# Kernel tuning notes

Hardware: AMD Instinct MI355X
Metric: run time of the kernel (lower is better)

## Reference

```python
import jax, jax.numpy as jnp
import numpy as np

N_NODES = 100000
N_EDGES = 1600000
IN_DIM, HID_DIM, OUT_DIM = 128, 128, 64


def setup_inputs() -> dict:
    key = jax.random.key(0)
    ks = jax.random.split(key, 8)
    x = jax.random.normal(ks[0], (N_NODES, IN_DIM), dtype=jnp.float32)
    edge_index = jax.random.randint(ks[1], (2, N_EDGES), 0, N_NODES, dtype=jnp.int64)
    s1 = 1.0 / np.sqrt(IN_DIM)
    s2 = 1.0 / np.sqrt(HID_DIM)
    return {
        "x": x,
        "edge_index": edge_index,
        "W1l": jax.random.normal(ks[2], (IN_DIM, HID_DIM), dtype=jnp.float32) * s1,
        "b1": jnp.zeros((HID_DIM,), dtype=jnp.float32),
        "W1r": jax.random.normal(ks[3], (IN_DIM, HID_DIM), dtype=jnp.float32) * s1,
        "W2l": jax.random.normal(ks[4], (HID_DIM, OUT_DIM), dtype=jnp.float32) * s2,
        "b2": jnp.zeros((OUT_DIM,), dtype=jnp.float32),
        "W2r": jax.random.normal(ks[5], (HID_DIM, OUT_DIM), dtype=jnp.float32) * s2,
    }


def _sage_conv(h, src, dst, n_nodes, Wl, bl, Wr):
    # mean-aggregate neighbor messages src -> dst, then linear + root linear
    msg = h[src]                                               # [E, d]
    summed = jax.ops.segment_sum(msg, dst, num_segments=n_nodes)
    cnt = jax.ops.segment_sum(jnp.ones((src.shape[0],), h.dtype), dst,
                              num_segments=n_nodes)
    aggr = summed / jnp.maximum(cnt, 1.0)[:, None]             # [N, d]
    return aggr @ Wl + bl + h @ Wr                             # [N, d_out]


def reference(x, edge_index, W1l, b1, W1r, W2l, b2, W2r):
    src, dst = edge_index[0], edge_index[1]
    n = x.shape[0]
    h = jax.nn.relu(_sage_conv(x, src, dst, n, W1l, b1, W1r))
    # dropout is identity in eval mode (training=False)
    return _sage_conv(h, src, dst, n, W2l, b2, W2r)
```

## Files before the change

kernel.cpp:

```cpp
#include <hip/hip_runtime.h>
#include <hip/hip_bf16.h>
#include <stdint.h>

#define N_NODES 100000
#define N_EDGES 1600000
#define IN_DIM 128
#define HID_DIM 128
#define OUT_DIM 64
#define NBUCKET 391
#define NBE 391
#define ECHUNK 4096
#define HM (NBUCKET * NBE)
#define NB_SCAN 150
#define SENTINEL N_NODES
#define PCAP 6144
#define GEMM_ROWBLKS 782
#define GEMM_GRID (GEMM_ROWBLKS * 2)

typedef __bf16 bf16x8 __attribute__((ext_vector_type(8)));
typedef float f32x4 __attribute__((ext_vector_type(4)));
typedef float f32x2 __attribute__((ext_vector_type(2)));

__device__ __forceinline__ uint16_t f_to_bf16(float f) {
    uint32_t u = __float_as_uint(f);
    u += 0x7fffu + ((u >> 16) & 1u);
    return (uint16_t)(u >> 16);
}
__device__ __forceinline__ uint32_t pack_bf16x2(float lo, float hi) {
    return (uint32_t)f_to_bf16(lo) | ((uint32_t)f_to_bf16(hi) << 16);
}


__global__ __launch_bounds__(256) void prep_k(const int* __restrict__ dst,
                                              const float* __restrict__ x,
                                              const float* __restrict__ W1l,
                                              const float* __restrict__ W1r,
                                              const float* __restrict__ W2l,
                                              const float* __restrict__ W2r,
                                              int* __restrict__ hist,
                                              uint32_t* __restrict__ xf8,
                                              uint16_t* __restrict__ wT1,
                                              uint16_t* __restrict__ wT2) {
    __shared__ int lh[NBUCKET];
    int blk = blockIdx.x, t = threadIdx.x;
    if (blk < NBE) {
        for (int i = t; i < NBUCKET; i += 256) lh[i] = 0;
        __syncthreads();
        int e0 = blk * ECHUNK;
        int e1 = e0 + ECHUNK; if (e1 > N_EDGES) e1 = N_EDGES;
        for (int e = e0 + t; e < e1; e += 256) atomicAdd(&lh[dst[e] >> 8], 1);
        __syncthreads();
        for (int i = t; i < NBUCKET; i += 256) hist[i * NBE + blk] = lh[i];
    } else if (blk < NBE + 6250) {
        int i = (blk - NBE) * 256 + t;
        if (blk == NBE && t < 32) xf8[N_NODES * 32 + t] = 0u;
        if (i >= N_NODES * IN_DIM / 8) return;
        const float4* xv = (const float4*)x;
        float4 v0 = xv[2 * i], v1 = xv[2 * i + 1];
        int p0 = __builtin_amdgcn_cvt_pk_fp8_f32(v0.x, v0.y, 0, false);
        p0 = __builtin_amdgcn_cvt_pk_fp8_f32(v0.z, v0.w, p0, true);
        int p1 = __builtin_amdgcn_cvt_pk_fp8_f32(v1.x, v1.y, 0, false);
        p1 = __builtin_amdgcn_cvt_pk_fp8_f32(v1.z, v1.w, p1, true);
        uint2 w2; w2.x = (uint32_t)p0; w2.y = (uint32_t)p1;
        ((uint2*)xf8)[i] = w2;
    } else {
        int i = (blk - NBE - 6250) * 256 + t;
        if (i < 128 * 256) {
            int n = i >> 8, k = i & 255;
            float v = (k < 128) ? W1l[k * 128 + n] : W1r[(k - 128) * 128 + n];
            wT1[i] = f_to_bf16(v);
        } else {
            int j = i - 128 * 256;
            if (j < 128 * 128) {
                int n = j >> 7, k = j & 127;
                float v = (n < 64) ? W2l[k * 64 + n] : W2r[k * 64 + (n - 64)];
                wT2[j] = f_to_bf16(v);
            }
        }
    }
}


__global__ void scan1_k(int* __restrict__ data, int* __restrict__ partials, int n) {
    __shared__ int sm[256];
    int tid = threadIdx.x;
    int base = blockIdx.x * 1024 + tid * 4;
    int v0 = 0, v1 = 0, v2 = 0, v3 = 0;
    if (base + 0 < n) v0 = data[base + 0];
    if (base + 1 < n) v1 = data[base + 1];
    if (base + 2 < n) v2 = data[base + 2];
    if (base + 3 < n) v3 = data[base + 3];
    int tot = v0 + v1 + v2 + v3;
    sm[tid] = tot;
    __syncthreads();
    int val = tot;
    for (int off = 1; off < 256; off <<= 1) {
        int x = (tid >= off) ? sm[tid - off] : 0;
        __syncthreads();
        val += x;
        sm[tid] = val;
        __syncthreads();
    }
    int excl = val - tot;
    if (tid == 255) partials[blockIdx.x] = val;
    if (base + 0 < n) data[base + 0] = excl;
    if (base + 1 < n) data[base + 1] = excl + v0;
    if (base + 2 < n) data[base + 2] = excl + v0 + v1;
    if (base + 3 < n) data[base + 3] = excl + v0 + v1 + v2;
}

__global__ void scan3_k(int* __restrict__ data, const int* __restrict__ partials, int n) {
    __shared__ int sm[256];
    __shared__ int sp[256];
    int t = threadIdx.x;
    int v = (t < NB_SCAN) ? partials[t] : 0;
    sm[t] = v;
    __syncthreads();
    int val = v;
    for (int off = 1; off < 256; off <<= 1) {
        int x = (t >= off) ? sm[t - off] : 0;
        __syncthreads();
        val += x;
        sm[t] = val;
        __syncthreads();
    }
    sp[t] = val - v;
    __syncthreads();
    int i = blockIdx.x * 256 + t;
    if (i < n) data[i] += sp[i >> 10];
}

__global__ __launch_bounds__(256) void scatter2_k(const int* __restrict__ src,
                                                  const int* __restrict__ dst,
                                                  const int* __restrict__ hoff,
                                                  uint32_t* __restrict__ packed) {
    __shared__ int loff[NBUCKET];
    int blk = blockIdx.x, t = threadIdx.x;
    for (int i = t; i < NBUCKET; i += 256) loff[i] = hoff[i * NBE + blk];
    __syncthreads();
    int e0 = blk * ECHUNK;
    int e1 = e0 + ECHUNK; if (e1 > N_EDGES) e1 = N_EDGES;
    for (int e = e0 + t; e < e1; e += 256) {
        int d = dst[e];
        int pos = atomicAdd(&loff[d >> 8], 1);
        packed[pos] = ((uint32_t)src[e] << 8) | (uint32_t)(d & 255);
    }
}


__global__ __launch_bounds__(256) void finalize_k(const uint32_t* __restrict__ packed,
                                                  const int* __restrict__ hoff,
                                                  int* __restrict__ csr,
                                                  int* __restrict__ deg,
                                                  int* __restrict__ prowst) {
    __shared__ int lhist[256];
    __shared__ int ssc[256];
    __shared__ int lcur[256];
    __shared__ int s_pcnt;
    __shared__ uint32_t lpk[PCAP];
    __shared__ int lcsr[PCAP];
    int b = blockIdx.x, t = threadIdx.x;
    int base = hoff[b * NBE];
    int next = (b + 1 < NBUCKET) ? hoff[(b + 1) * NBE] : N_EDGES;
    int cnt = next - base;
    lhist[t] = 0;
    __syncthreads();
    bool fit = (cnt <= PCAP);
    if (fit) {
        for (int i = t; i < cnt; i += 256) {
            uint32_t pk = packed[base + i];
            lpk[i] = pk;
            atomicAdd(&lhist[pk & 255u], 1);
        }
    } else {
        for (int i = t; i < cnt; i += 256) atomicAdd(&lhist[packed[base + i] & 255u], 1);
    }
    __syncthreads();
    int d = lhist[t];
    int pd = (d + 7) & ~7;
    ssc[t] = pd;
    __syncthreads();
    int val = pd;
    for (int off = 1; off < 256; off <<= 1) {
        int x = (t >= off) ? ssc[t - off] : 0;
        __syncthreads();
        val += x;
        ssc[t] = val;
        __syncthreads();
    }
    int excl = val - pd;
    lcur[t] = excl;
    if (t == 255) s_pcnt = val;
    int node = (b << 8) + t;
    if (node < N_NODES) { deg[node] = d; prowst[node] = b * PCAP + excl; }
    __syncthreads();
    int pcnt = s_pcnt;
    int cbase = b * PCAP;
    if (fit && pcnt <= PCAP) {
        for (int i = t; i < pcnt; i += 256) lcsr[i] = SENTINEL;
        __syncthreads();
        for (int i = t; i < cnt; i += 256) {
            uint32_t pk = lpk[i];
            int pos = atomicAdd(&lcur[pk & 255u], 1);
            lcsr[pos] = (int)(pk >> 8);
        }
        __syncthreads();
        for (int i = t; i < pcnt; i += 256) csr[cbase + i] = lcsr[i];
    } else {
        int lim = pcnt < PCAP ? pcnt : PCAP;
        for (int i = t; i < lim; i += 256) csr[cbase + i] = SENTINEL;
        __syncthreads();
        for (int i = t; i < cnt; i += 256) {
            uint32_t pk = packed[base + i];
            int pos = atomicAdd(&lcur[pk & 255u], 1);
            if (pos < PCAP) csr[cbase + pos] = (int)(pk >> 8);
        }
    }
}


__global__ void aggregate_k(const int* __restrict__ csr, const int* __restrict__ prowst,
                            const int* __restrict__ deg,
                            const uint32_t* __restrict__ inf8, uint32_t* __restrict__ out2) {
    int gw = (blockIdx.x * blockDim.x + threadIdx.x) >> 6;
    int lane = threadIdx.x & 63;
    int c = lane & 31, p = lane >> 5;
    int node = 2 * gw + p;
    int start = prowst[node];
    int d = deg[node];
    int pd = (d + 7) & ~7;
    f32x2 s01 = (f32x2){0.f, 0.f}, s23 = (f32x2){0.f, 0.f};
    for (int j = 0; j < pd; j += 8) {
        uint32_t q[8];
#pragma unroll
        for (int u = 0; u < 8; u++) {
            int s = csr[start + j + u];
            q[u] = inf8[(s << 5) + c];
        }
#pragma unroll
        for (int u = 0; u < 8; u++) {
            s01 += __builtin_amdgcn_cvt_pk_f32_fp8((int)q[u], false);
            s23 += __builtin_amdgcn_cvt_pk_f32_fp8((int)q[u], true);
        }
    }
    float inv = 1.0f / (float)(d > 0 ? d : 1);
    uint2 o;
    o.x = pack_bf16x2(s01[0] * inv, s01[1] * inv);
    o.y = pack_bf16x2(s23[0] * inv, s23[1] * inv);
    ((uint2*)out2)[node * 32 + c] = o;
}


__global__ __launch_bounds__(256, 4) void gemm1_k(const uint16_t* __restrict__ ab,
                                                  const float* __restrict__ x,
                                                  const uint16_t* __restrict__ wT1,
                                                  const float* __restrict__ b1,
                                                  uint16_t* __restrict__ hb) {
    __shared__ uint16_t lw[64 * 256];
    int t = threadIdx.x;
    int nh = blockIdx.x & 1;
    int rowblk = blockIdx.x >> 1;
    {
        const uint4* gsrc = (const uint4*)wT1;
        uint4* ldst = (uint4*)lw;
        for (int i = t; i < 2048; i += 256) {
            int r = i >> 5, cc = i & 31;
            ldst[(r << 5) + (cc ^ (r & 31))] = gsrc[((nh * 64 + r) << 5) + cc];
        }
    }
    __syncthreads();

    int wave = t >> 6;
    int lane = t & 63;
    int m0 = rowblk * 128 + wave * 32;
    int mr = lane & 15, quad = lane >> 4;

    const uint16_t* A1[2];
    const float* A2[2];
#pragma unroll
    for (int s = 0; s < 2; s++) {
        int row = m0 + s * 16 + mr;
        if (row > N_NODES - 1) row = N_NODES - 1;
        A1[s] = ab + (size_t)row * 128 + quad * 8;
        A2[s] = x + (size_t)row * 128 + quad * 8;
    }

    f32x4 acc[4][2];
#pragma unroll
    for (int nt = 0; nt < 4; nt++)
#pragma unroll
        for (int s = 0; s < 2; s++) acc[nt][s] = (f32x4){0.f, 0.f, 0.f, 0.f};

#pragma unroll
    for (int kt = 0; kt < 8; kt++) {
        bf16x8 av[2];
#pragma unroll
        for (int s = 0; s < 2; s++) {
            if (kt < 4) {
                av[s] = *reinterpret_cast<const bf16x8*>(A1[s] + kt * 32);
            } else {
                const float* ap = A2[s] + (kt - 4) * 32;
                float4 f0 = *reinterpret_cast<const float4*>(ap);
                float4 f1 = *reinterpret_cast<const float4*>(ap + 4);
                union { uint16_t u[8]; bf16x8 v; } cv;
                cv.u[0] = f_to_bf16(f0.x); cv.u[1] = f_to_bf16(f0.y);
                cv.u[2] = f_to_bf16(f0.z); cv.u[3] = f_to_bf16(f0.w);
                cv.u[4] = f_to_bf16(f1.x); cv.u[5] = f_to_bf16(f1.y);
                cv.u[6] = f_to_bf16(f1.z); cv.u[7] = f_to_bf16(f1.w);
                av[s] = cv.v;
            }
        }
#pragma unroll
        for (int nt = 0; nt < 4; nt++) {
            int brow = nt * 16 + mr;
            int chunk = kt * 4 + quad;
            const uint16_t* bp = lw + (brow << 8) + ((chunk ^ (brow & 31)) << 3);
            bf16x8 b = *reinterpret_cast<const bf16x8*>(bp);
#pragma unroll
            for (int s = 0; s < 2; s++)
                acc[nt][s] = __builtin_amdgcn_mfma_f32_16x16x32_bf16(av[s], b, acc[nt][s], 0, 0, 0);
        }
    }

    __syncthreads();
#pragma unroll
    for (int nt = 0; nt < 4; nt++) {
        int col = nt * 16 + mr;
        float bias = b1[nh * 64 + col];
#pragma unroll
        for (int s = 0; s < 2; s++) {
#pragma unroll
            for (int r = 0; r < 4; r++) {
                int lrow = wave * 32 + s * 16 + quad * 4 + r;
                float v = acc[nt][s][r] + bias;
                v = v > 0.f ? v : 0.f;
                lw[lrow * 72 + col] = f_to_bf16(v);
            }
        }
    }
    __syncthreads();
    {
        int rows0 = rowblk * 128;
        for (int c2 = t; c2 < 1024; c2 += 256) {
            int r = c2 >> 3, part = c2 & 7;
            int grow = rows0 + r;
            if (grow < N_NODES) {
                uint4 v = *reinterpret_cast<const uint4*>(lw + r * 72 + part * 8);
                *reinterpret_cast<uint4*>(hb + (size_t)grow * 128 + nh * 64 + part * 8) = v;
            }
        }
    }
}


__global__ __launch_bounds__(256, 4) void gemm2_k(const uint16_t* __restrict__ hb,
                                                  const uint16_t* __restrict__ wT2,
                                                  const float* __restrict__ b2,
                                                  uint8_t* __restrict__ g,
                                                  float* __restrict__ z) {
    __shared__ uint16_t lw[64 * 128];
    int t = threadIdx.x;
    int nh = blockIdx.x & 1;
    int rowblk = blockIdx.x >> 1;
    if (blockIdx.x == 0 && t < 16)
        ((uint32_t*)(g + (size_t)N_NODES * 64))[t] = 0u;
    {
        const uint4* gsrc = (const uint4*)wT2;
        uint4* ldst = (uint4*)lw;
        for (int i = t; i < 1024; i += 256) {
            int r = i >> 4, cc = i & 15;
            ldst[(r << 4) + (cc ^ (r & 15))] = gsrc[((nh * 64 + r) << 4) + cc];
        }
    }
    __syncthreads();

    int wave = t >> 6;
    int lane = t & 63;
    int m0 = rowblk * 128 + wave * 32;
    int mr = lane & 15, quad = lane >> 4;

    const uint16_t* A[2];
#pragma unroll
    for (int s = 0; s < 2; s++) {
        int row = m0 + s * 16 + mr;
        if (row > N_NODES - 1) row = N_NODES - 1;
        A[s] = hb + (size_t)row * 128 + quad * 8;
    }

    f32x4 acc[4][2];
#pragma unroll
    for (int nt = 0; nt < 4; nt++)
#pragma unroll
        for (int s = 0; s < 2; s++) acc[nt][s] = (f32x4){0.f, 0.f, 0.f, 0.f};

#pragma unroll
    for (int kt = 0; kt < 4; kt++) {
        bf16x8 av[2];
#pragma unroll
        for (int s = 0; s < 2; s++)
            av[s] = *reinterpret_cast<const bf16x8*>(A[s] + kt * 32);
#pragma unroll
        for (int nt = 0; nt < 4; nt++) {
            int brow = nt * 16 + mr;
            int chunk = kt * 4 + quad;
            const uint16_t* bp = lw + (brow << 7) + ((chunk ^ (brow & 15)) << 3);
            bf16x8 b = *reinterpret_cast<const bf16x8*>(bp);
#pragma unroll
            for (int s = 0; s < 2; s++)
                acc[nt][s] = __builtin_amdgcn_mfma_f32_16x16x32_bf16(av[s], b, acc[nt][s], 0, 0, 0);
        }
    }

    if (nh == 0) {
        __syncthreads();
        uint8_t* ep8 = (uint8_t*)lw;
#pragma unroll
        for (int nt = 0; nt < 4; nt++) {
            int col = nt * 16 + mr;
#pragma unroll
            for (int s = 0; s < 2; s++) {
#pragma unroll
                for (int r = 0; r < 4; r++) {
                    int lrow = wave * 32 + s * 16 + quad * 4 + r;
                    float v = acc[nt][s][r];
                    int pk = __builtin_amdgcn_cvt_pk_fp8_f32(v, v, 0, false);
                    ep8[lrow * 80 + col] = (uint8_t)(pk & 0xff);
                }
            }
        }
        __syncthreads();
        int rows0 = rowblk * 128;
        for (int c2 = t; c2 < 512; c2 += 256) {
            int r = c2 >> 2, part = c2 & 3;
            int grow = rows0 + r;
            if (grow < N_NODES) {
                uint4 v = *reinterpret_cast<const uint4*>(ep8 + r * 80 + part * 16);
                *reinterpret_cast<uint4*>(g + (size_t)grow * 64 + part * 16) = v;
            }
        }
    } else {
#pragma unroll
        for (int nt = 0; nt < 4; nt++) {
            int col = nt * 16 + mr;
            float bias = b2[col];
#pragma unroll
            for (int s = 0; s < 2; s++) {
#pragma unroll
                for (int r = 0; r < 4; r++) {
                    int row = m0 + s * 16 + quad * 4 + r;
                    if (row < N_NODES)
                        z[(size_t)row * 64 + col] = acc[nt][s][r] + bias;
                }
            }
        }
    }
}


__global__ void agg2_k(const int* __restrict__ csr, const int* __restrict__ prowst,
                       const int* __restrict__ deg,
                       const uint32_t* __restrict__ g4, const float* __restrict__ z,
                       float* __restrict__ out) {
    int gw = (blockIdx.x * blockDim.x + threadIdx.x) >> 6;
    int lane = threadIdx.x & 63;
    int c = lane & 15, q4 = lane >> 4;
    int node = 4 * gw + q4;
    int start = prowst[node];
    int d = deg[node];
    int pd = (d + 7) & ~7;
    f32x2 s01 = (f32x2){0.f, 0.f}, s23 = (f32x2){0.f, 0.f};
    for (int j = 0; j < pd; j += 8) {
        uint32_t q[8];
#pragma unroll
        for (int u = 0; u < 8; u++) {
            int s = csr[start + j + u];
            q[u] = g4[(s << 4) + c];
        }
#pragma unroll
        for (int u = 0; u < 8; u++) {
            s01 += __builtin_amdgcn_cvt_pk_f32_fp8((int)q[u], false);
            s23 += __builtin_amdgcn_cvt_pk_f32_fp8((int)q[u], true);
        }
    }
    float inv = 1.0f / (float)(d > 0 ? d : 1);
    float4 zz = ((const float4*)z)[node * 16 + c];
    float4 o;
    o.x = s01[0] * inv + zz.x;
    o.y = s01[1] * inv + zz.y;
    o.z = s23[0] * inv + zz.z;
    o.w = s23[1] * inv + zz.w;
    ((float4*)out)[node * 16 + c] = o;
}


extern "C" void kernel_launch(void* const* d_in, const int* in_sizes, int n_in,
                              void* d_out, int out_size, void* d_ws, size_t ws_size,
                              hipStream_t stream) {
    const float* x   = (const float*)d_in[0];
    const int*  ei   = (const int*)d_in[1];
    const float* W1l = (const float*)d_in[2];
    const float* b1  = (const float*)d_in[3];
    const float* W1r = (const float*)d_in[4];
    const float* W2l = (const float*)d_in[5];
    const float* b2  = (const float*)d_in[6];
    const float* W2r = (const float*)d_in[7];
    float* out = (float*)d_out;

    const int* srcv = ei;
    const int* dstv = ei + N_EDGES;

    char* ws = (char*)d_ws;
    int*      deg      = (int*)(ws + 0);
    int*      prowst   = (int*)(ws + 401408);
    int*      partials = (int*)(ws + 802816);
    int*      csr      = (int*)(ws + 1209344);
    uint16_t* wT1      = (uint16_t*)(ws + 13809664);
    uint16_t* wT2      = (uint16_t*)(ws + 13875200);
    uint8_t*  g        = (uint8_t*)(ws + 13907968);
    char*     abreg    = (ws + 39507968);
    uint16_t* hb       = (uint16_t*)(ws + 65107968);
    uint16_t* ab       = (uint16_t*)abreg;
    float*    z        = (float*)abreg;
    uint32_t* packed   = (uint32_t*)hb;
    int*      hoff     = (int*)(ws + 65107968 + 6400000);
    uint32_t* xf8      = (uint32_t*)(ws + 65107968 + 7013376);

    prep_k<<<NBE + 6250 + 192, 256, 0, stream>>>(dstv, x, W1l, W1r, W2l, W2r,
                                                 hoff, xf8, wT1, wT2);
    scan1_k<<<NB_SCAN, 256, 0, stream>>>(hoff, partials, HM);
    scan3_k<<<(HM + 255) / 256, 256, 0, stream>>>(hoff, partials, HM);
    scatter2_k<<<NBE, 256, 0, stream>>>(srcv, dstv, hoff, packed);
    finalize_k<<<NBUCKET, 256, 0, stream>>>(packed, hoff, csr, deg, prowst);

    aggregate_k<<<12500, 256, 0, stream>>>(csr, prowst, deg, xf8, (uint32_t*)ab);
    gemm1_k<<<GEMM_GRID, 256, 0, stream>>>(ab, x, wT1, b1, hb);

    gemm2_k<<<GEMM_GRID, 256, 0, stream>>>(hb, wT2, b2, g, z);
    agg2_k<<<6250, 256, 0, stream>>>(csr, prowst, deg, (const uint32_t*)g, z, out);
}
```

Measured before the change: 163.5 us.

## Fuse both layer GEMMs into one kernel, keeping hidden activations in LDS

Merges gemm1_k and gemm2_k into a single gemm12_k. Each block computes the full 128-wide ReLU hidden tile for its 128 rows into a swizzled LDS buffer, then runs the second-layer GEMM for all 128 output columns (fp8 neighbor messages plus fp32 root term) straight from LDS. This removes the global write and re-read of the bf16 hidden matrix and one kernel launch. In exchange each block uses about 64KB of LDS, holds more accumulators, runs at lower occupancy (launch bounds 2), and the grid shrinks to half as many blocks.

```diff
diff --git a/kernel.cpp b/kernel.cpp
--- a/kernel.cpp
+++ b/kernel.cpp
@@ -15,7 +15,6 @@
 #define SENTINEL N_NODES
 #define PCAP 6144
 #define GEMM_ROWBLKS 782
-#define GEMM_GRID (GEMM_ROWBLKS * 2)
 
 typedef __bf16 bf16x8 __attribute__((ext_vector_type(8)));
 typedef float f32x4 __attribute__((ext_vector_type(4)));
@@ -251,24 +250,20 @@
 }
 
 
-__global__ __launch_bounds__(256, 4) void gemm1_k(const uint16_t* __restrict__ ab,
-                                                  const float* __restrict__ x,
-                                                  const uint16_t* __restrict__ wT1,
-                                                  const float* __restrict__ b1,
-                                                  uint16_t* __restrict__ hb) {
-    __shared__ uint16_t lw[64 * 256];
+__global__ __launch_bounds__(256, 2) void gemm12_k(const uint16_t* __restrict__ ab,
+                                                   const float* __restrict__ x,
+                                                   const uint16_t* __restrict__ wT1,
+                                                   const float* __restrict__ b1,
+                                                   const uint16_t* __restrict__ wT2,
+                                                   const float* __restrict__ b2,
+                                                   uint8_t* __restrict__ g,
+                                                   float* __restrict__ z) {
+    __shared__ uint16_t lwA[64 * 256];
+    __shared__ uint16_t lhb[128 * 128];
     int t = threadIdx.x;
-    int nh = blockIdx.x & 1;
-    int rowblk = blockIdx.x >> 1;
-    {
-        const uint4* gsrc = (const uint4*)wT1;
-        uint4* ldst = (uint4*)lw;
-        for (int i = t; i < 2048; i += 256) {
-            int r = i >> 5, cc = i & 31;
-            ldst[(r << 5) + (cc ^ (r & 31))] = gsrc[((nh * 64 + r) << 5) + cc];
-        }
-    }
-    __syncthreads();
+    int rowblk = blockIdx.x;
+    if (rowblk == 0 && t < 16)
+        ((uint32_t*)(g + (size_t)N_NODES * 64))[t] = 0u;
 
     int wave = t >> 6;
     int lane = t & 63;
@@ -285,135 +280,128 @@
         A2[s] = x + (size_t)row * 128 + quad * 8;
     }
 
-    f32x4 acc[4][2];
-#pragma unroll
-    for (int nt = 0; nt < 4; nt++)
-#pragma unroll
-        for (int s = 0; s < 2; s++) acc[nt][s] = (f32x4){0.f, 0.f, 0.f, 0.f};
-
-#pragma unroll
-    for (int kt = 0; kt < 8; kt++) {
+    for (int nh = 0; nh < 2; nh++) {
+        {
+            const uint4* gsrc = (const uint4*)wT1;
+            uint4* ldst = (uint4*)lwA;
+            for (int i = t; i < 2048; i += 256) {
+                int r = i >> 5, cc = i & 31;
+                ldst[(r << 5) + (cc ^ (r & 31))] = gsrc[((nh * 64 + r) << 5) + cc];
+            }
+        }
+        __syncthreads();
+
+        f32x4 acc[4][2];
+#pragma unroll
+        for (int nt = 0; nt < 4; nt++)
+#pragma unroll
+            for (int s = 0; s < 2; s++) acc[nt][s] = (f32x4){0.f, 0.f, 0.f, 0.f};
+
+#pragma unroll
+        for (int kt = 0; kt < 8; kt++) {
+            bf16x8 av[2];
+#pragma unroll
+            for (int s = 0; s < 2; s++) {
+                if (kt < 4) {
+                    av[s] = *reinterpret_cast<const bf16x8*>(A1[s] + kt * 32);
+                } else {
+                    const float* ap = A2[s] + (kt - 4) * 32;
+                    float4 f0 = *reinterpret_cast<const float4*>(ap);
+                    float4 f1 = *reinterpret_cast<const float4*>(ap + 4);
+                    union { uint16_t u[8]; bf16x8 v; } cv;
+                    cv.u[0] = f_to_bf16(f0.x); cv.u[1] = f_to_bf16(f0.y);
+                    cv.u[2] = f_to_bf16(f0.z); cv.u[3] = f_to_bf16(f0.w);
+                    cv.u[4] = f_to_bf16(f1.x); cv.u[5] = f_to_bf16(f1.y);
+                    cv.u[6] = f_to_bf16(f1.z); cv.u[7] = f_to_bf16(f1.w);
+                    av[s] = cv.v;
+                }
+            }
+#pragma unroll
+            for (int nt = 0; nt < 4; nt++) {
+                int brow = nt * 16 + mr;
+                int chunk = kt * 4 + quad;
+                const uint16_t* bp = lwA + (brow << 8) + ((chunk ^ (brow & 31)) << 3);
+                bf16x8 b = *reinterpret_cast<const bf16x8*>(bp);
+#pragma unroll
+                for (int s = 0; s < 2; s++)
+                    acc[nt][s] = __builtin_amdgcn_mfma_f32_16x16x32_bf16(av[s], b, acc[nt][s], 0, 0, 0);
+            }
+        }
+        __syncthreads();
+
+#pragma unroll
+        for (int nt = 0; nt < 4; nt++) {
+            int col = nh * 64 + nt * 16 + mr;
+            float bias = b1[col];
+            int c2 = col >> 3, clo = col & 7;
+#pragma unroll
+            for (int s = 0; s < 2; s++) {
+#pragma unroll
+                for (int r = 0; r < 4; r++) {
+                    int lrow = wave * 32 + s * 16 + quad * 4 + r;
+                    float v = acc[nt][s][r] + bias;
+                    v = v > 0.f ? v : 0.f;
+                    lhb[(lrow << 7) + ((c2 ^ (lrow & 15)) << 3) + clo] = f_to_bf16(v);
+                }
+            }
+        }
+    }
+
+    {
+        const uint4* gsrc = (const uint4*)wT2;
+        uint4* ldst = (uint4*)lwA;
+        for (int i = t; i < 2048; i += 256) {
+            int r = i >> 4, cc = i & 15;
+            ldst[(r << 4) + (cc ^ (r & 15))] = gsrc[(r << 4) + cc];
+        }
+    }
+    __syncthreads();
+
+    f32x4 acc2[8][2];
+#pragma unroll
+    for (int nt = 0; nt < 8; nt++)
+#pragma unroll
+        for (int s = 0; s < 2; s++) acc2[nt][s] = (f32x4){0.f, 0.f, 0.f, 0.f};
+
+#pragma unroll
+    for (int kt = 0; kt < 4; kt++) {
         bf16x8 av[2];
 #pragma unroll
         for (int s = 0; s < 2; s++) {
-            if (kt < 4) {
-                av[s] = *reinterpret_cast<const bf16x8*>(A1[s] + kt * 32);
-            } else {
-                const float* ap = A2[s] + (kt - 4) * 32;
-                float4 f0 = *reinterpret_cast<const float4*>(ap);
-                float4 f1 = *reinterpret_cast<const float4*>(ap + 4);
-                union { uint16_t u[8]; bf16x8 v; } cv;
-                cv.u[0] = f_to_bf16(f0.x); cv.u[1] = f_to_bf16(f0.y);
-                cv.u[2] = f_to_bf16(f0.z); cv.u[3] = f_to_bf16(f0.w);
-                cv.u[4] = f_to_bf16(f1.x); cv.u[5] = f_to_bf16(f1.y);
-                cv.u[6] = f_to_bf16(f1.z); cv.u[7] = f_to_bf16(f1.w);
-                av[s] = cv.v;
-            }
-        }
-#pragma unroll
-        for (int nt = 0; nt < 4; nt++) {
+            int row = wave * 32 + s * 16 + mr;
+            int chunk = kt * 4 + quad;
+            const uint16_t* ap = lhb + (row << 7) + ((chunk ^ (row & 15)) << 3);
+            av[s] = *reinterpret_cast<const bf16x8*>(ap);
+        }
+#pragma unroll
+        for (int nt = 0; nt < 8; nt++) {
             int brow = nt * 16 + mr;
             int chunk = kt * 4 + quad;
-            const uint16_t* bp = lw + (brow << 8) + ((chunk ^ (brow & 31)) << 3);
+            const uint16_t* bp = lwA + (brow << 7) + ((chunk ^ (brow & 15)) << 3);
             bf16x8 b = *reinterpret_cast<const bf16x8*>(bp);
 #pragma unroll
             for (int s = 0; s < 2; s++)
-                acc[nt][s] = __builtin_amdgcn_mfma_f32_16x16x32_bf16(av[s], b, acc[nt][s], 0, 0, 0);
-        }
-    }
-
-    __syncthreads();
-#pragma unroll
-    for (int nt = 0; nt < 4; nt++) {
-        int col = nt * 16 + mr;
-        float bias = b1[nh * 64 + col];
+                acc2[nt][s] = __builtin_amdgcn_mfma_f32_16x16x32_bf16(av[s], b, acc2[nt][s], 0, 0, 0);
+        }
+    }
+
+#pragma unroll
+    for (int nt = 4; nt < 8; nt++) {
+        int zcol = nt * 16 + mr - 64;
+        float bias = b2[zcol];
 #pragma unroll
         for (int s = 0; s < 2; s++) {
 #pragma unroll
             for (int r = 0; r < 4; r++) {
-                int lrow = wave * 32 + s * 16 + quad * 4 + r;
-                float v = acc[nt][s][r] + bias;
-                v = v > 0.f ? v : 0.f;
-                lw[lrow * 72 + col] = f_to_bf16(v);
+                int row = m0 + s * 16 + quad * 4 + r;
+                if (row < N_NODES)
+                    z[(size_t)row * 64 + zcol] = acc2[nt][s][r] + bias;
             }
         }
     }
     __syncthreads();
     {
-        int rows0 = rowblk * 128;
-        for (int c2 = t; c2 < 1024; c2 += 256) {
-            int r = c2 >> 3, part = c2 & 7;
-            int grow = rows0 + r;
-            if (grow < N_NODES) {
-                uint4 v = *reinterpret_cast<const uint4*>(lw + r * 72 + part * 8);
-                *reinterpret_cast<uint4*>(hb + (size_t)grow * 128 + nh * 64 + part * 8) = v;
-            }
-        }
-    }
-}
-
-
-__global__ __launch_bounds__(256, 4) void gemm2_k(const uint16_t* __restrict__ hb,
-                                                  const uint16_t* __restrict__ wT2,
-                                                  const float* __restrict__ b2,
-                                                  uint8_t* __restrict__ g,
-                                                  float* __restrict__ z) {
-    __shared__ uint16_t lw[64 * 128];
-    int t = threadIdx.x;
-    int nh = blockIdx.x & 1;
-    int rowblk = blockIdx.x >> 1;
-    if (blockIdx.x == 0 && t < 16)
-        ((uint32_t*)(g + (size_t)N_NODES * 64))[t] = 0u;
-    {
-        const uint4* gsrc = (const uint4*)wT2;
-        uint4* ldst = (uint4*)lw;
-        for (int i = t; i < 1024; i += 256) {
-            int r = i >> 4, cc = i & 15;
-            ldst[(r << 4) + (cc ^ (r & 15))] = gsrc[((nh * 64 + r) << 4) + cc];
-        }
-    }
-    __syncthreads();
-
-    int wave = t >> 6;
-    int lane = t & 63;
-    int m0 = rowblk * 128 + wave * 32;
-    int mr = lane & 15, quad = lane >> 4;
-
-    const uint16_t* A[2];
-#pragma unroll
-    for (int s = 0; s < 2; s++) {
-        int row = m0 + s * 16 + mr;
-        if (row > N_NODES - 1) row = N_NODES - 1;
-        A[s] = hb + (size_t)row * 128 + quad * 8;
-    }
-
-    f32x4 acc[4][2];
-#pragma unroll
-    for (int nt = 0; nt < 4; nt++)
-#pragma unroll
-        for (int s = 0; s < 2; s++) acc[nt][s] = (f32x4){0.f, 0.f, 0.f, 0.f};
-
-#pragma unroll
-    for (int kt = 0; kt < 4; kt++) {
-        bf16x8 av[2];
-#pragma unroll
-        for (int s = 0; s < 2; s++)
-            av[s] = *reinterpret_cast<const bf16x8*>(A[s] + kt * 32);
-#pragma unroll
-        for (int nt = 0; nt < 4; nt++) {
-            int brow = nt * 16 + mr;
-            int chunk = kt * 4 + quad;
-            const uint16_t* bp = lw + (brow << 7) + ((chunk ^ (brow & 15)) << 3);
-            bf16x8 b = *reinterpret_cast<const bf16x8*>(bp);
-#pragma unroll
-            for (int s = 0; s < 2; s++)
-                acc[nt][s] = __builtin_amdgcn_mfma_f32_16x16x32_bf16(av[s], b, acc[nt][s], 0, 0, 0);
-        }
-    }
-
-    if (nh == 0) {
-        __syncthreads();
-        uint8_t* ep8 = (uint8_t*)lw;
+        uint8_t* ep8 = (uint8_t*)lwA;
 #pragma unroll
         for (int nt = 0; nt < 4; nt++) {
             int col = nt * 16 + mr;
@@ -422,7 +410,7 @@
 #pragma unroll
                 for (int r = 0; r < 4; r++) {
                     int lrow = wave * 32 + s * 16 + quad * 4 + r;
-                    float v = acc[nt][s][r];
+                    float v = acc2[nt][s][r];
                     int pk = __builtin_amdgcn_cvt_pk_fp8_f32(v, v, 0, false);
                     ep8[lrow * 80 + col] = (uint8_t)(pk & 0xff);
                 }
@@ -436,21 +424,6 @@
             if (grow < N_NODES) {
                 uint4 v = *reinterpret_cast<const uint4*>(ep8 + r * 80 + part * 16);
                 *reinterpret_cast<uint4*>(g + (size_t)grow * 64 + part * 16) = v;
-            }
-        }
-    } else {
-#pragma unroll
-        for (int nt = 0; nt < 4; nt++) {
-            int col = nt * 16 + mr;
-            float bias = b2[col];
-#pragma unroll
-            for (int s = 0; s < 2; s++) {
-#pragma unroll
-                for (int r = 0; r < 4; r++) {
-                    int row = m0 + s * 16 + quad * 4 + r;
-                    if (row < N_NODES)
-                        z[(size_t)row * 64 + col] = acc[nt][s][r] + bias;
-                }
             }
         }
     }
@@ -518,10 +491,9 @@
     uint16_t* wT2      = (uint16_t*)(ws + 13875200);
     uint8_t*  g        = (uint8_t*)(ws + 13907968);
     char*     abreg    = (ws + 39507968);
-    uint16_t* hb       = (uint16_t*)(ws + 65107968);
     uint16_t* ab       = (uint16_t*)abreg;
     float*    z        = (float*)abreg;
-    uint32_t* packed   = (uint32_t*)hb;
+    uint32_t* packed   = (uint32_t*)(ws + 65107968);
     int*      hoff     = (int*)(ws + 65107968 + 6400000);
     uint32_t* xf8      = (uint32_t*)(ws + 65107968 + 7013376);
 
@@ -533,8 +505,6 @@
     finalize_k<<<NBUCKET, 256, 0, stream>>>(packed, hoff, csr, deg, prowst);
 
     aggregate_k<<<12500, 256, 0, stream>>>(csr, prowst, deg, xf8, (uint32_t*)ab);
-    gemm1_k<<<GEMM_GRID, 256, 0, stream>>>(ab, x, wT1, b1, hb);
-
-    gemm2_k<<<GEMM_GRID, 256, 0, stream>>>(hb, wT2, b2, g, z);
+    gemm12_k<<<GEMM_ROWBLKS, 256, 0, stream>>>(ab, x, wT1, b1, wT2, b2, g, z);
     agg2_k<<<6250, 256, 0, stream>>>(csr, prowst, deg, (const uint32_t*)g, z, out);
 }
```

Result: faster. 153.4 us (median of 2 runs) (-6.2%).
